# Kernel optimization log

Hardware: AMD Instinct MI355X
Metric: run time of the kernel (lower is better)

## Reference

```python
import jax, jax.numpy as jnp
import numpy as np


def setup_inputs() -> dict:
    key = jax.random.key(0)
    B, S, H, D = 4, 2048, 16, 64
    qkv = jax.random.normal(key, (B, S, 3, H, D), dtype=jnp.float32)
    return {"qkv": qkv}


def reference(qkv):
    # qkv: (B, S, 3, H, d). Eval mode -> dropout is identity.
    B, S, _, H, D = qkv.shape
    q = jnp.transpose(qkv[:, :, 0], (0, 2, 1, 3))  # (B,H,S,d)
    k = jnp.transpose(qkv[:, :, 1], (0, 2, 1, 3))
    v = jnp.transpose(qkv[:, :, 2], (0, 2, 1, 3))
    scale = D ** -0.5
    scores = jnp.einsum("bhqd,bhkd->bhqk", q, k) * scale  # (B,H,S,S)
    causal = jnp.tril(jnp.ones((S, S), dtype=bool))
    scores = jnp.where(causal[None, None], scores, -jnp.inf)
    attn = jax.nn.softmax(scores, axis=-1)
    out = jnp.einsum("bhqk,bhkd->bhqd", attn, v)  # (B,H,S,d)
    return out
```

## Files before the change

### kernel.cpp

```cpp
#include <hip/hip_runtime.h>
#include <hip/hip_bf16.h>


#define S_LEN 2048
#define NHEAD 16
#define DHEAD 64
#define CHUNK 64
#define KVBLK 64
#define NQB   (S_LEN / CHUNK)
#define NPAIR (NQB / 2)
#define SROW  3072
#define KOFF  1024
#define VOFF  2048
#define PPIT  72

typedef __attribute__((ext_vector_type(8))) short bf16x8;
typedef __attribute__((ext_vector_type(4))) float f32x4;

__device__ __forceinline__ short f2bf(float f) {
    union { __hip_bfloat16 b; short s; } u;
    u.b = __float2bfloat16(f);
    return u.s;
}
__device__ __forceinline__ short f2bf_trunc(float f) {
    union { float f; unsigned int u; } v;
    v.f = f;
    return (short)(v.u >> 16);
}
__device__ __forceinline__ unsigned int pack2(float lo, float hi) {
    return (unsigned int)(unsigned short)f2bf(lo) | ((unsigned int)(unsigned short)f2bf(hi) << 16);
}
__device__ __forceinline__ void gl_lds16(const short* g, short* l) {
    __builtin_amdgcn_global_load_lds(
        (const __attribute__((address_space(1))) void*)g,
        (__attribute__((address_space(3))) void*)l, 16, 0, 0);
}
__device__ __forceinline__ float fexp2(float x) {
    float r;
    asm("v_exp_f32 %0, %1" : "=v"(r) : "v"(x));
    return r;
}

__global__ __launch_bounds__(256)
void prepass_kernel(const float* __restrict__ qkv,
                    short* __restrict__ kws, short* __restrict__ vtws)
{
    __shared__ float lds_t[64][65];

    const int tid = threadIdx.x;
    const int bh  = blockIdx.x >> 5;
    const int s0  = (blockIdx.x & 31) * 64;

    const float* qkv_bh = qkv + (size_t)(bh >> 4) * (S_LEN * SROW) + (bh & 15) * DHEAD;
    short* kws_bh = kws  + (size_t)bh * (S_LEN * DHEAD);
    short* vt_bh  = vtws + (size_t)bh * (S_LEN * DHEAD);

    const int row = tid >> 2;
    const int cq  = (tid & 3) * 16;

    {
        const float* kp = qkv_bh + (size_t)(s0 + row) * SROW + KOFF + cq;
        f32x4 a = *(const f32x4*)kp,       b = *(const f32x4*)(kp + 4);
        f32x4 c = *(const f32x4*)(kp + 8), d = *(const f32x4*)(kp + 12);
        bf16x8 w0, w1;
        #pragma unroll
        for (int j = 0; j < 4; ++j) {
            w0[j] = f2bf(a[j]); w0[4 + j] = f2bf(b[j]);
            w1[j] = f2bf(c[j]); w1[4 + j] = f2bf(d[j]);
        }
        *(bf16x8*)&kws_bh[(size_t)(s0 + row) * 64 + cq]     = w0;
        *(bf16x8*)&kws_bh[(size_t)(s0 + row) * 64 + cq + 8] = w1;
    }
    {
        const float* vp = qkv_bh + (size_t)(s0 + row) * SROW + VOFF + cq;
        f32x4 a = *(const f32x4*)vp,       b = *(const f32x4*)(vp + 4);
        f32x4 c = *(const f32x4*)(vp + 8), d = *(const f32x4*)(vp + 12);
        #pragma unroll
        for (int j = 0; j < 4; ++j) {
            lds_t[row][cq + j]      = a[j];
            lds_t[row][cq + 4 + j]  = b[j];
            lds_t[row][cq + 8 + j]  = c[j];
            lds_t[row][cq + 12 + j] = d[j];
        }
    }
    __syncthreads();
    {
        const int d = row, sq = cq;
        bf16x8 w0, w1;
        #pragma unroll
        for (int j = 0; j < 8; ++j) {
            w0[j] = f2bf(lds_t[sq + j][d]);
            w1[j] = f2bf(lds_t[sq + 8 + j][d]);
        }
        *(bf16x8*)&vt_bh[(size_t)d * S_LEN + s0 + sq]     = w0;
        *(bf16x8*)&vt_bh[(size_t)d * S_LEN + s0 + sq + 8] = w1;
    }
}

__global__ __launch_bounds__(256)
void attn_fwd_ws(const float* __restrict__ qkv,
                 const short* __restrict__ kws, const short* __restrict__ vtws,
                 float* __restrict__ out)
{
    __shared__ __attribute__((aligned(16))) short lds_k [KVBLK * 64];
    __shared__ __attribute__((aligned(16))) short lds_vt[2][DHEAD * 64];
    __shared__ __attribute__((aligned(16))) short lds_p [4][16][PPIT];

    const int tid  = threadIdx.x;
    const int wave = tid >> 6;
    const int lane = tid & 63;
    const int l16  = lane & 15;
    const int lg   = lane >> 4;
    const int lr8  = lane >> 3;
    const int lc8  = lane & 7;
    const int swz  = (lc8 * 8) ^ (lr8 << 3);
    const int rsw  = (l16 & 7) << 3;

    const int bid = blockIdx.x;
    const int pr  = bid & 15;
    const int bh  = bid >> 4;

    const float* qkv_bh = qkv + (size_t)(bh >> 4) * (S_LEN * SROW) + (bh & 15) * DHEAD;
    const short* kws_bh = kws  + (size_t)bh * (S_LEN * DHEAD);
    const short* vt_bh  = vtws + (size_t)bh * (S_LEN * DHEAD);

    const int qbA = pr;
    const int qbB = NQB - 1 - pr;
    const int qloA = qbA * CHUNK + wave * 16;
    const int qloB = qbB * CHUNK + wave * 16;

    short* pwr = &lds_p[wave][lg * 4][l16];
    const short* prd = &lds_p[wave][l16][lg * 8];

    {
        #pragma unroll
        for (int i = 0; i < 2; ++i) {
            const int row = i * 32 + wave * 8 + lr8;
            gl_lds16(&kws_bh[(size_t)row * 64 + swz],    &lds_k    [i * 2048 + wave * 512]);
            gl_lds16(&vt_bh [(size_t)row * S_LEN + swz], &lds_vt[0][i * 2048 + wave * 512]);
        }
    }

    const float qscale = 0.125f * 1.44269504088896f;
    bf16x8 qf[2][2];
    #pragma unroll
    for (int m = 0; m < 2; ++m) {
        const int qrow = (m == 0 ? qloA : qloB) + l16;
        #pragma unroll
        for (int ks = 0; ks < 2; ++ks) {
            const float* qp = qkv_bh + (size_t)qrow * SROW + ks * 32 + lg * 8;
            f32x4 a = *(const f32x4*)qp;
            f32x4 c = *(const f32x4*)(qp + 4);
            bf16x8 v;
            #pragma unroll
            for (int j = 0; j < 4; ++j) { v[j] = f2bf(a[j] * qscale); v[4 + j] = f2bf(c[j] * qscale); }
            qf[m][ks] = v;
        }
    }

    bf16x8 onesf;
    #pragma unroll
    for (int j = 0; j < 8; ++j) onesf[j] = (short)0x3F80;

    f32x4 o[2][4];
    f32x4 lsum[2];
    float m_r[2][4];
    #pragma unroll
    for (int m = 0; m < 2; ++m) {
        #pragma unroll
        for (int n = 0; n < 4; ++n) o[m][n] = (f32x4){0.f, 0.f, 0.f, 0.f};
        lsum[m] = (f32x4){0.f, 0.f, 0.f, 0.f};
        #pragma unroll
        for (int r = 0; r < 4; ++r) m_r[m][r] = -1e30f;
    }

    __syncthreads();

    const int ntiles = qbB + 1;
    int cur = 0;

    for (int it = 0; it < ntiles; ++it) {
        const int kv0 = it * KVBLK;
        const bool actA = (kv0 <= qloA + 15);

        f32x4 s[2][4];
        #pragma unroll
        for (int m = 0; m < 2; ++m)
            #pragma unroll
            for (int c = 0; c < 4; ++c) s[m][c] = (f32x4){0.f, 0.f, 0.f, 0.f};
        #pragma unroll
        for (int ks = 0; ks < 2; ++ks) {
            #pragma unroll
            for (int c = 0; c < 4; ++c) {
                bf16x8 kf = *(const bf16x8*)&lds_k[(c * 16 + l16) * 64 + ((ks * 32 + lg * 8) ^ rsw)];
                s[1][c] = __builtin_amdgcn_mfma_f32_16x16x32_bf16(qf[1][ks], kf, s[1][c], 0, 0, 0);
                if (actA)
                    s[0][c] = __builtin_amdgcn_mfma_f32_16x16x32_bf16(qf[0][ks], kf, s[0][c], 0, 0, 0);
            }
        }

        __syncthreads();

        if (it + 1 < ntiles) {
            const int kn = kv0 + KVBLK;
            #pragma unroll
            for (int i = 0; i < 2; ++i) {
                const int row = i * 32 + wave * 8 + lr8;
                gl_lds16(&kws_bh[(size_t)(kn + row) * 64 + swz],  &lds_k          [i * 2048 + wave * 512]);
                gl_lds16(&vt_bh [(size_t)row * S_LEN + kn + swz], &lds_vt[cur ^ 1][i * 2048 + wave * 512]);
            }
        }

        #pragma unroll
        for (int mi = 0; mi < 2; ++mi) {
            const int m = 1 - mi;
            if (m == 0 && !actA) continue;
            const int qlo_m = (m == 0) ? qloA : qloB;

            if (kv0 + KVBLK - 1 > qlo_m) {
                #pragma unroll
                for (int r = 0; r < 4; ++r) {
                    const int qg = qlo_m + lg * 4 + r;
                    #pragma unroll
                    for (int c = 0; c < 4; ++c)
                        if (kv0 + c * 16 + l16 > qg) s[m][c][r] = -1e30f;
                }
            }

            float lmax[4];
            #pragma unroll
            for (int r = 0; r < 4; ++r)
                lmax[r] = fmaxf(fmaxf(s[m][0][r], s[m][1][r]), fmaxf(s[m][2][r], s[m][3][r]));

            const int okflag = (lmax[0] <= m_r[m][0] + 11.54f) && (lmax[1] <= m_r[m][1] + 11.54f) &&
                               (lmax[2] <= m_r[m][2] + 11.54f) && (lmax[3] <= m_r[m][3] + 11.54f);
            if (!__all(okflag)) {
                #pragma unroll
                for (int r = 0; r < 4; ++r) {
                    float mt = lmax[r];
                    mt = fmaxf(mt, __shfl_xor(mt, 1));
                    mt = fmaxf(mt, __shfl_xor(mt, 2));
                    mt = fmaxf(mt, __shfl_xor(mt, 4));
                    mt = fmaxf(mt, __shfl_xor(mt, 8));
                    const float mn    = fmaxf(m_r[m][r], mt);
                    const float alpha = fexp2(m_r[m][r] - mn);
                    m_r[m][r] = mn;
                    lsum[m][r] *= alpha;
                    #pragma unroll
                    for (int n = 0; n < 4; ++n) o[m][n][r] *= alpha;
                }
            }

            #pragma unroll
            for (int c = 0; c < 4; ++c) {
                #pragma unroll
                for (int r = 0; r < 4; ++r) {
                    const float p = fexp2(s[m][c][r] - m_r[m][r]);
                    pwr[r * PPIT + c * 16] = f2bf_trunc(p);
                }
            }
            asm volatile("s_waitcnt lgkmcnt(0)" ::: "memory");
            __builtin_amdgcn_sched_barrier(0);

            __builtin_amdgcn_s_setprio(1);
            #pragma unroll
            for (int ks = 0; ks < 2; ++ks) {
                bf16x8 pa = *(const bf16x8*)&prd[ks * 32];
                lsum[m] = __builtin_amdgcn_mfma_f32_16x16x32_bf16(pa, onesf, lsum[m], 0, 0, 0);
                #pragma unroll
                for (int n = 0; n < 4; ++n) {
                    bf16x8 vf = *(const bf16x8*)&lds_vt[cur][(n * 16 + l16) * 64 + ((ks * 32 + lg * 8) ^ rsw)];
                    o[m][n] = __builtin_amdgcn_mfma_f32_16x16x32_bf16(pa, vf, o[m][n], 0, 0, 0);
                }
            }
            __builtin_amdgcn_s_setprio(0);
        }
        __syncthreads();
        cur ^= 1;
    }

    #pragma unroll
    for (int m = 0; m < 2; ++m) {
        const int qlo_m = (m == 0) ? qloA : qloB;
        float* outp = out + ((size_t)bh * S_LEN + qlo_m) * DHEAD;
        #pragma unroll
        for (int r = 0; r < 4; ++r) {
            const float inv = 1.0f / lsum[m][r];
            #pragma unroll
            for (int n = 0; n < 4; ++n)
                outp[(lg * 4 + r) * DHEAD + n * 16 + l16] = o[m][n][r] * inv;
        }
    }
}

#define KP 72
#define VP 72
#define PP 76
__global__ __launch_bounds__(256)
void attn_fwd_fallback(const float* __restrict__ qkv, float* __restrict__ out)
{
    __shared__ __attribute__((aligned(16))) short lds_k [KVBLK * KP];
    __shared__ __attribute__((aligned(16))) short lds_vt[DHEAD * VP];
    __shared__ __attribute__((aligned(16))) short lds_p [4 * 32 * PP];

    const int tid  = threadIdx.x;
    const int wave = tid >> 6;
    const int lane = tid & 63;
    const int l16  = lane & 15;
    const int lg   = lane >> 4;

    const int bid = blockIdx.x;
    const int pr  = bid & 15;
    const int bh  = bid >> 4;

    const float* qkv_bh = qkv + (size_t)(bh >> 4) * (S_LEN * SROW) + (bh & 15) * DHEAD;
    const int qbA = pr;
    const int qbB = NQB - 1 - pr;
    const int qloA = qbA * CHUNK + wave * 16;
    const int qloB = qbB * CHUNK + wave * 16;

    bf16x8 qf[2][2];
    #pragma unroll
    for (int m = 0; m < 2; ++m) {
        const int qrow = (m == 0 ? qloA : qloB) + l16;
        #pragma unroll
        for (int ks = 0; ks < 2; ++ks) {
            const float* qp = qkv_bh + (size_t)qrow * SROW + ks * 32 + lg * 8;
            f32x4 a = *(const f32x4*)qp;
            f32x4 c = *(const f32x4*)(qp + 4);
            bf16x8 v;
            #pragma unroll
            for (int j = 0; j < 4; ++j) { v[j] = f2bf(a[j] * 0.125f); v[4 + j] = f2bf(c[j] * 0.125f); }
            qf[m][ks] = v;
        }
    }

    f32x4 o[2][4];
    float m_r[2][4], l_r[2][4];
    #pragma unroll
    for (int m = 0; m < 2; ++m)
        #pragma unroll
        for (int n = 0; n < 4; ++n) o[m][n] = (f32x4){0.f, 0.f, 0.f, 0.f};
    #pragma unroll
    for (int m = 0; m < 2; ++m)
        #pragma unroll
        for (int r = 0; r < 4; ++r) { m_r[m][r] = -1e30f; l_r[m][r] = 0.f; }

    const int st_kr = tid >> 2;
    const int st_kc = (tid & 3) * 16;
    const int st_vp = tid & 31;
    const int st_vd = (tid >> 5) * 8;

    f32x4 pk[4], pv[4];
    const int ntiles = qbB + 1;
    {
        const float* kp = qkv_bh + (size_t)st_kr * SROW + KOFF + st_kc;
        pk[0] = *(const f32x4*)kp;       pk[1] = *(const f32x4*)(kp + 4);
        pk[2] = *(const f32x4*)(kp + 8); pk[3] = *(const f32x4*)(kp + 12);
        const float* vp = qkv_bh + (size_t)(2 * st_vp) * SROW + VOFF + st_vd;
        pv[0] = *(const f32x4*)vp;           pv[1] = *(const f32x4*)(vp + 4);
        pv[2] = *(const f32x4*)(vp + SROW);  pv[3] = *(const f32x4*)(vp + SROW + 4);
    }

    for (int it = 0; it < ntiles; ++it) {
        const int kv0 = it * KVBLK;
        {
            bf16x8 w0, w1;
            #pragma unroll
            for (int j = 0; j < 4; ++j) {
                w0[j] = f2bf(pk[0][j]); w0[4 + j] = f2bf(pk[1][j]);
                w1[j] = f2bf(pk[2][j]); w1[4 + j] = f2bf(pk[3][j]);
            }
            *(bf16x8*)&lds_k[st_kr * KP + st_kc]     = w0;
            *(bf16x8*)&lds_k[st_kr * KP + st_kc + 8] = w1;
            #pragma unroll
            for (int i = 0; i < 4; ++i) {
                *(unsigned int*)&lds_vt[(st_vd + i)     * VP + 2 * st_vp] = pack2(pv[0][i], pv[2][i]);
                *(unsigned int*)&lds_vt[(st_vd + 4 + i) * VP + 2 * st_vp] = pack2(pv[1][i], pv[3][i]);
            }
        }
        __syncthreads();
        if (it + 1 < ntiles) {
            const int kn = kv0 + KVBLK;
            const float* kp = qkv_bh + (size_t)(kn + st_kr) * SROW + KOFF + st_kc;
            pk[0] = *(const f32x4*)kp;       pk[1] = *(const f32x4*)(kp + 4);
            pk[2] = *(const f32x4*)(kp + 8); pk[3] = *(const f32x4*)(kp + 12);
            const float* vp = qkv_bh + (size_t)(kn + 2 * st_vp) * SROW + VOFF + st_vd;
            pv[0] = *(const f32x4*)vp;           pv[1] = *(const f32x4*)(vp + 4);
            pv[2] = *(const f32x4*)(vp + SROW);  pv[3] = *(const f32x4*)(vp + SROW + 4);
        }
        const bool actA = (kv0 <= qloA + 15);
        f32x4 s[2][4];
        #pragma unroll
        for (int m = 0; m < 2; ++m)
            #pragma unroll
            for (int c = 0; c < 4; ++c) s[m][c] = (f32x4){0.f, 0.f, 0.f, 0.f};
        #pragma unroll
        for (int ks = 0; ks < 2; ++ks) {
            #pragma unroll
            for (int c = 0; c < 4; ++c) {
                bf16x8 kf = *(const bf16x8*)&lds_k[(c * 16 + l16) * KP + ks * 32 + lg * 8];
                s[1][c] = __builtin_amdgcn_mfma_f32_16x16x32_bf16(qf[1][ks], kf, s[1][c], 0, 0, 0);
                if (actA)
                    s[0][c] = __builtin_amdgcn_mfma_f32_16x16x32_bf16(qf[0][ks], kf, s[0][c], 0, 0, 0);
            }
        }
        short* pw = &lds_p[wave * 32 * PP];
        #pragma unroll
        for (int m = 0; m < 2; ++m) {
            if (m == 0 && !actA) continue;
            const int qlo_m = (m == 0) ? qloA : qloB;
            if (kv0 + KVBLK - 1 > qlo_m) {
                #pragma unroll
                for (int r = 0; r < 4; ++r) {
                    const int qg = qlo_m + lg * 4 + r;
                    #pragma unroll
                    for (int c = 0; c < 4; ++c)
                        if (kv0 + c * 16 + l16 > qg) s[m][c][r] = -1e30f;
                }
            }
            #pragma unroll
            for (int r = 0; r < 4; ++r) {
                float mt = fmaxf(fmaxf(s[m][0][r], s[m][1][r]), fmaxf(s[m][2][r], s[m][3][r]));
                mt = fmaxf(mt, __shfl_xor(mt, 1));
                mt = fmaxf(mt, __shfl_xor(mt, 2));
                mt = fmaxf(mt, __shfl_xor(mt, 4));
                mt = fmaxf(mt, __shfl_xor(mt, 8));
                const float mn    = fmaxf(m_r[m][r], mt);
                const float alpha = __expf(m_r[m][r] - mn);
                m_r[m][r] = mn;
                float p0 = __expf(s[m][0][r] - mn);
                float p1 = __expf(s[m][1][r] - mn);
                float p2 = __expf(s[m][2][r] - mn);
                float p3 = __expf(s[m][3][r] - mn);
                float rs = (p0 + p1) + (p2 + p3);
                rs += __shfl_xor(rs, 1);
                rs += __shfl_xor(rs, 2);
                rs += __shfl_xor(rs, 4);
                rs += __shfl_xor(rs, 8);
                l_r[m][r] = l_r[m][r] * alpha + rs;
                #pragma unroll
                for (int n = 0; n < 4; ++n) o[m][n][r] *= alpha;
                const int prow = m * 16 + lg * 4 + r;
                pw[prow * PP +      l16] = f2bf(p0);
                pw[prow * PP + 16 + l16] = f2bf(p1);
                pw[prow * PP + 32 + l16] = f2bf(p2);
                pw[prow * PP + 48 + l16] = f2bf(p3);
            }
        }
        asm volatile("s_waitcnt lgkmcnt(0)" ::: "memory");
        __builtin_amdgcn_sched_barrier(0);
        #pragma unroll
        for (int ks = 0; ks < 2; ++ks) {
            bf16x8 pa1 = *(const bf16x8*)&pw[(16 + l16) * PP + ks * 32 + lg * 8];
            #pragma unroll
            for (int n = 0; n < 4; ++n) {
                bf16x8 vf = *(const bf16x8*)&lds_vt[(n * 16 + l16) * VP + ks * 32 + lg * 8];
                o[1][n] = __builtin_amdgcn_mfma_f32_16x16x32_bf16(pa1, vf, o[1][n], 0, 0, 0);
            }
            if (actA) {
                bf16x8 pa0 = *(const bf16x8*)&pw[l16 * PP + ks * 32 + lg * 8];
                #pragma unroll
                for (int n = 0; n < 4; ++n) {
                    bf16x8 vf = *(const bf16x8*)&lds_vt[(n * 16 + l16) * VP + ks * 32 + lg * 8];
                    o[0][n] = __builtin_amdgcn_mfma_f32_16x16x32_bf16(pa0, vf, o[0][n], 0, 0, 0);
                }
            }
        }
        __syncthreads();
    }
    #pragma unroll
    for (int m = 0; m < 2; ++m) {
        const int qlo_m = (m == 0) ? qloA : qloB;
        float* outp = out + ((size_t)bh * S_LEN + qlo_m) * DHEAD;
        #pragma unroll
        for (int r = 0; r < 4; ++r) {
            const float inv = 1.0f / l_r[m][r];
            #pragma unroll
            for (int n = 0; n < 4; ++n)
                outp[(lg * 4 + r) * DHEAD + n * 16 + l16] = o[m][n][r] * inv;
        }
    }
}

extern "C" void kernel_launch(void* const* d_in, const int* in_sizes, int n_in,
                              void* d_out, int out_size, void* d_ws, size_t ws_size,
                              hipStream_t stream) {
    const float* qkv = (const float*)d_in[0];
    float* out = (float*)d_out;
    const size_t need = (size_t)2 * 64 * S_LEN * DHEAD * sizeof(short);
    const int nblocks = NPAIR * 4 * NHEAD;
    if (ws_size >= need) {
        short* kws  = (short*)d_ws;
        short* vtws = kws + (size_t)64 * S_LEN * DHEAD;
        prepass_kernel<<<dim3(64 * 32), dim3(256), 0, stream>>>(qkv, kws, vtws);
        attn_fwd_ws<<<dim3(nblocks), dim3(256), 0, stream>>>(qkv, kws, vtws, out);
    } else {
        attn_fwd_fallback<<<dim3(nblocks), dim3(256), 0, stream>>>(qkv, out);
    }
}
```

Measured before the change: 116.5 us.

## Process paired query blocks sequentially instead of sharing K/V tiles

Each workgroup used to handle two query chunks (pr and its mirror) in one pass over the K/V tiles, so every loaded K/V tile fed both chunks. The kernel now runs two separate phases, one per chunk, each reloading its own K/V range. This halves the live accumulator registers, which may allow better occupancy or scheduling. In exchange, K/V tiles for the overlapping prefix are loaded from global memory twice, adding traffic and extra barrier iterations.

```diff
diff --git a/kernel.cpp b/kernel.cpp
--- a/kernel.cpp
+++ b/kernel.cpp
@@ -124,116 +124,97 @@
     const short* kws_bh = kws  + (size_t)bh * (S_LEN * DHEAD);
     const short* vt_bh  = vtws + (size_t)bh * (S_LEN * DHEAD);
 
-    const int qbA = pr;
-    const int qbB = NQB - 1 - pr;
-    const int qloA = qbA * CHUNK + wave * 16;
-    const int qloB = qbB * CHUNK + wave * 16;
-
     short* pwr = &lds_p[wave][lg * 4][l16];
     const short* prd = &lds_p[wave][l16][lg * 8];
 
-    {
-        #pragma unroll
-        for (int i = 0; i < 2; ++i) {
-            const int row = i * 32 + wave * 8 + lr8;
-            gl_lds16(&kws_bh[(size_t)row * 64 + swz],    &lds_k    [i * 2048 + wave * 512]);
-            gl_lds16(&vt_bh [(size_t)row * S_LEN + swz], &lds_vt[0][i * 2048 + wave * 512]);
-        }
-    }
-
     const float qscale = 0.125f * 1.44269504088896f;
-    bf16x8 qf[2][2];
+
+    bf16x8 onesf;
     #pragma unroll
-    for (int m = 0; m < 2; ++m) {
-        const int qrow = (m == 0 ? qloA : qloB) + l16;
+    for (int j = 0; j < 8; ++j) onesf[j] = (short)0x3F80;
+
+    for (int ph = 0; ph < 2; ++ph) {
+        const int qb  = (ph == 0) ? pr : (NQB - 1 - pr);
+        const int qlo = qb * CHUNK + wave * 16;
+
+        bf16x8 qf[2];
         #pragma unroll
         for (int ks = 0; ks < 2; ++ks) {
-            const float* qp = qkv_bh + (size_t)qrow * SROW + ks * 32 + lg * 8;
+            const float* qp = qkv_bh + (size_t)(qlo + l16) * SROW + ks * 32 + lg * 8;
             f32x4 a = *(const f32x4*)qp;
             f32x4 c = *(const f32x4*)(qp + 4);
             bf16x8 v;
             #pragma unroll
             for (int j = 0; j < 4; ++j) { v[j] = f2bf(a[j] * qscale); v[4 + j] = f2bf(c[j] * qscale); }
-            qf[m][ks] = v;
-        }
-    }
-
-    bf16x8 onesf;
-    #pragma unroll
-    for (int j = 0; j < 8; ++j) onesf[j] = (short)0x3F80;
-
-    f32x4 o[2][4];
-    f32x4 lsum[2];
-    float m_r[2][4];
-    #pragma unroll
-    for (int m = 0; m < 2; ++m) {
-        #pragma unroll
-        for (int n = 0; n < 4; ++n) o[m][n] = (f32x4){0.f, 0.f, 0.f, 0.f};
-        lsum[m] = (f32x4){0.f, 0.f, 0.f, 0.f};
-        #pragma unroll
-        for (int r = 0; r < 4; ++r) m_r[m][r] = -1e30f;
-    }
-
-    __syncthreads();
-
-    const int ntiles = qbB + 1;
-    int cur = 0;
-
-    for (int it = 0; it < ntiles; ++it) {
-        const int kv0 = it * KVBLK;
-        const bool actA = (kv0 <= qloA + 15);
-
-        f32x4 s[2][4];
-        #pragma unroll
-        for (int m = 0; m < 2; ++m)
-            #pragma unroll
-            for (int c = 0; c < 4; ++c) s[m][c] = (f32x4){0.f, 0.f, 0.f, 0.f};
-        #pragma unroll
-        for (int ks = 0; ks < 2; ++ks) {
-            #pragma unroll
-            for (int c = 0; c < 4; ++c) {
-                bf16x8 kf = *(const bf16x8*)&lds_k[(c * 16 + l16) * 64 + ((ks * 32 + lg * 8) ^ rsw)];
-                s[1][c] = __builtin_amdgcn_mfma_f32_16x16x32_bf16(qf[1][ks], kf, s[1][c], 0, 0, 0);
-                if (actA)
-                    s[0][c] = __builtin_amdgcn_mfma_f32_16x16x32_bf16(qf[0][ks], kf, s[0][c], 0, 0, 0);
-            }
-        }
-
-        __syncthreads();
-
-        if (it + 1 < ntiles) {
-            const int kn = kv0 + KVBLK;
+            qf[ks] = v;
+        }
+
+        f32x4 o[4];
+        f32x4 lsum;
+        float m_r[4];
+        #pragma unroll
+        for (int n = 0; n < 4; ++n) o[n] = (f32x4){0.f, 0.f, 0.f, 0.f};
+        lsum = (f32x4){0.f, 0.f, 0.f, 0.f};
+        #pragma unroll
+        for (int r = 0; r < 4; ++r) m_r[r] = -1e30f;
+
+        {
             #pragma unroll
             for (int i = 0; i < 2; ++i) {
                 const int row = i * 32 + wave * 8 + lr8;
-                gl_lds16(&kws_bh[(size_t)(kn + row) * 64 + swz],  &lds_k          [i * 2048 + wave * 512]);
-                gl_lds16(&vt_bh [(size_t)row * S_LEN + kn + swz], &lds_vt[cur ^ 1][i * 2048 + wave * 512]);
-            }
-        }
-
-        #pragma unroll
-        for (int mi = 0; mi < 2; ++mi) {
-            const int m = 1 - mi;
-            if (m == 0 && !actA) continue;
-            const int qlo_m = (m == 0) ? qloA : qloB;
-
-            if (kv0 + KVBLK - 1 > qlo_m) {
+                gl_lds16(&kws_bh[(size_t)row * 64 + swz],    &lds_k    [i * 2048 + wave * 512]);
+                gl_lds16(&vt_bh [(size_t)row * S_LEN + swz], &lds_vt[0][i * 2048 + wave * 512]);
+            }
+        }
+        __syncthreads();
+
+        int cur = 0;
+        const int ntiles = qb + 1;
+
+        for (int it = 0; it < ntiles; ++it) {
+            const int kv0 = it * KVBLK;
+
+            f32x4 s[4];
+            #pragma unroll
+            for (int c = 0; c < 4; ++c) s[c] = (f32x4){0.f, 0.f, 0.f, 0.f};
+            #pragma unroll
+            for (int ks = 0; ks < 2; ++ks) {
+                #pragma unroll
+                for (int c = 0; c < 4; ++c) {
+                    bf16x8 kf = *(const bf16x8*)&lds_k[(c * 16 + l16) * 64 + ((ks * 32 + lg * 8) ^ rsw)];
+                    s[c] = __builtin_amdgcn_mfma_f32_16x16x32_bf16(qf[ks], kf, s[c], 0, 0, 0);
+                }
+            }
+
+            __syncthreads();
+
+            if (it + 1 < ntiles) {
+                const int kn = kv0 + KVBLK;
+                #pragma unroll
+                for (int i = 0; i < 2; ++i) {
+                    const int row = i * 32 + wave * 8 + lr8;
+                    gl_lds16(&kws_bh[(size_t)(kn + row) * 64 + swz],  &lds_k          [i * 2048 + wave * 512]);
+                    gl_lds16(&vt_bh [(size_t)row * S_LEN + kn + swz], &lds_vt[cur ^ 1][i * 2048 + wave * 512]);
+                }
+            }
+
+            if (kv0 + KVBLK - 1 > qlo) {
                 #pragma unroll
                 for (int r = 0; r < 4; ++r) {
-                    const int qg = qlo_m + lg * 4 + r;
+                    const int qg = qlo + lg * 4 + r;
                     #pragma unroll
                     for (int c = 0; c < 4; ++c)
-                        if (kv0 + c * 16 + l16 > qg) s[m][c][r] = -1e30f;
+                        if (kv0 + c * 16 + l16 > qg) s[c][r] = -1e30f;
                 }
             }
 
             float lmax[4];
             #pragma unroll
             for (int r = 0; r < 4; ++r)
-                lmax[r] = fmaxf(fmaxf(s[m][0][r], s[m][1][r]), fmaxf(s[m][2][r], s[m][3][r]));
-
-            const int okflag = (lmax[0] <= m_r[m][0] + 11.54f) && (lmax[1] <= m_r[m][1] + 11.54f) &&
-                               (lmax[2] <= m_r[m][2] + 11.54f) && (lmax[3] <= m_r[m][3] + 11.54f);
+                lmax[r] = fmaxf(fmaxf(s[0][r], s[1][r]), fmaxf(s[2][r], s[3][r]));
+
+            const int okflag = (lmax[0] <= m_r[0] + 11.54f) && (lmax[1] <= m_r[1] + 11.54f) &&
+                               (lmax[2] <= m_r[2] + 11.54f) && (lmax[3] <= m_r[3] + 11.54f);
             if (!__all(okflag)) {
                 #pragma unroll
                 for (int r = 0; r < 4; ++r) {
@@ -242,12 +223,12 @@
                     mt = fmaxf(mt, __shfl_xor(mt, 2));
                     mt = fmaxf(mt, __shfl_xor(mt, 4));
                     mt = fmaxf(mt, __shfl_xor(mt, 8));
-                    const float mn    = fmaxf(m_r[m][r], mt);
-                    const float alpha = fexp2(m_r[m][r] - mn);
-                    m_r[m][r] = mn;
-                    lsum[m][r] *= alpha;
+                    const float mn    = fmaxf(m_r[r], mt);
+                    const float alpha = fexp2(m_r[r] - mn);
+                    m_r[r] = mn;
+                    lsum[r] *= alpha;
                     #pragma unroll
-                    for (int n = 0; n < 4; ++n) o[m][n][r] *= alpha;
+                    for (int n = 0; n < 4; ++n) o[n][r] *= alpha;
                 }
             }
 
@@ -255,7 +236,7 @@
             for (int c = 0; c < 4; ++c) {
                 #pragma unroll
                 for (int r = 0; r < 4; ++r) {
-                    const float p = fexp2(s[m][c][r] - m_r[m][r]);
+                    const float p = fexp2(s[c][r] - m_r[r]);
                     pwr[r * PPIT + c * 16] = f2bf_trunc(p);
                 }
             }
@@ -266,29 +247,26 @@
             #pragma unroll
             for (int ks = 0; ks < 2; ++ks) {
                 bf16x8 pa = *(const bf16x8*)&prd[ks * 32];
-                lsum[m] = __builtin_amdgcn_mfma_f32_16x16x32_bf16(pa, onesf, lsum[m], 0, 0, 0);
+                lsum = __builtin_amdgcn_mfma_f32_16x16x32_bf16(pa, onesf, lsum, 0, 0, 0);
                 #pragma unroll
                 for (int n = 0; n < 4; ++n) {
                     bf16x8 vf = *(const bf16x8*)&lds_vt[cur][(n * 16 + l16) * 64 + ((ks * 32 + lg * 8) ^ rsw)];
-                    o[m][n] = __builtin_amdgcn_mfma_f32_16x16x32_bf16(pa, vf, o[m][n], 0, 0, 0);
+                    o[n] = __builtin_amdgcn_mfma_f32_16x16x32_bf16(pa, vf, o[n], 0, 0, 0);
                 }
             }
             __builtin_amdgcn_s_setprio(0);
-        }
-        __syncthreads();
-        cur ^= 1;
-    }
-
-    #pragma unroll
-    for (int m = 0; m < 2; ++m) {
-        const int qlo_m = (m == 0) ? qloA : qloB;
-        float* outp = out + ((size_t)bh * S_LEN + qlo_m) * DHEAD;
+
+            __syncthreads();
+            cur ^= 1;
+        }
+
+        float* outp = out + ((size_t)bh * S_LEN + qlo) * DHEAD;
         #pragma unroll
         for (int r = 0; r < 4; ++r) {
-            const float inv = 1.0f / lsum[m][r];
+            const float inv = 1.0f / lsum[r];
             #pragma unroll
             for (int n = 0; n < 4; ++n)
-                outp[(lg * 4 + r) * DHEAD + n * 16 + l16] = o[m][n][r] * inv;
+                outp[(lg * 4 + r) * DHEAD + n * 16 + l16] = o[n][r] * inv;
         }
     }
 }
```

Measured after the change: 120.3 us. +3.2%, slower.
